# Performance work log

Measured on AMD Instinct MI355X. Metric: run time of the kernel, lower is better.

The kernel has to match this reference:

```python
import jax, jax.numpy as jnp
import numpy as np

N = 1048576          # total octree nodes across the batch
C = 64               # in_channels
BATCH_SIZE = 16
GROUP = 16           # clamped: min_group_channels(4)*group(32) > 64 -> group = 64//4
CPG = C // GROUP     # channels_per_group = 4
EPS = 1e-5


def setup_inputs() -> dict:
    key = jax.random.key(0)
    k1, k2, k3, k4 = jax.random.split(key, 4)
    data = jax.random.normal(k1, (N, C), dtype=jnp.float32)
    batch_id = jnp.sort(jax.random.randint(k2, (N,), 0, BATCH_SIZE)).astype(jnp.int32)
    weights = jax.random.normal(k3, (1, C), dtype=jnp.float32)
    bias = jax.random.normal(k4, (1, C), dtype=jnp.float32)
    return {"data": data, "batch_id": batch_id, "weights": weights, "bias": bias}


def _adjust_for_group(t):
    # sum over channels within each group, broadcast back to all channels
    if CPG > 1:
        t = t.reshape(-1, GROUP, CPG).sum(-1, keepdims=True)
        t = jnp.broadcast_to(t, (t.shape[0], GROUP, CPG)).reshape(-1, C)
    return t


def reference(data, batch_id, weights, bias):
    # per-sample element counts, scaled so the group-sum of means is a true group mean
    ones = jnp.ones((data.shape[0],), dtype=data.dtype)
    count = jax.ops.segment_sum(ones, batch_id, num_segments=BATCH_SIZE)[:, None]  # [B,1]
    count = count * CPG
    inv_count = 1.0 / (count + EPS)

    mean = jax.ops.segment_sum(data, batch_id, num_segments=BATCH_SIZE) * inv_count  # [B,C]
    mean = _adjust_for_group(mean)
    out = data - mean[batch_id]  # gather broadcast [N,C]

    var = jax.ops.segment_sum(out * out, batch_id, num_segments=BATCH_SIZE) * inv_count
    var = _adjust_for_group(var)
    inv_std = jax.lax.rsqrt(var + EPS)

    out = out * inv_std[batch_id]
    return out * weights + bias
```

## Files before the change

kernel.cpp:

```cpp
#include <hip/hip_runtime.h>

#define NBATCH 16
#define NCH 64
#define CPG 4
#define NGRP 16
#define EPSV 1e-5f

typedef float f32x4 __attribute__((ext_vector_type(4)));


__global__ void ogn_stats(const float* __restrict__ data,
                          const int* __restrict__ bid,
                          float* __restrict__ S1,
                          float* __restrict__ S2,
                          int* __restrict__ cnt,
                          int N, int rows_per_block) {
    __shared__ float ls1[NBATCH * NCH];
    __shared__ float ls2[NBATCH * NCH];
    __shared__ int   lcnt[NBATCH];

    for (int i = threadIdx.x; i < NBATCH * NCH; i += blockDim.x) {
        ls1[i] = 0.f;
        ls2[i] = 0.f;
    }
    if (threadIdx.x < NBATCH) lcnt[threadIdx.x] = 0;
    __syncthreads();

    const int t     = threadIdx.x;
    const int c4    = t & 15;
    const int rlane = t >> 4;

    long long row_begin = (long long)blockIdx.x * rows_per_block;
    long long row_end   = row_begin + rows_per_block;
    if (row_end > N) row_end = N;

    const float4* data4 = (const float4*)data;

    float4 s1 = make_float4(0.f, 0.f, 0.f, 0.f);
    float4 s2 = make_float4(0.f, 0.f, 0.f, 0.f);
    int cur = -1;
    int c   = 0;

#define FLUSH() do { if (cur >= 0) {                                   \
        int base_ = cur * NCH + c4 * 4;                                \
        atomicAdd(&ls1[base_ + 0], s1.x);                              \
        atomicAdd(&ls1[base_ + 1], s1.y);                              \
        atomicAdd(&ls1[base_ + 2], s1.z);                              \
        atomicAdd(&ls1[base_ + 3], s1.w);                              \
        atomicAdd(&ls2[base_ + 0], s2.x);                              \
        atomicAdd(&ls2[base_ + 1], s2.y);                              \
        atomicAdd(&ls2[base_ + 2], s2.z);                              \
        atomicAdd(&ls2[base_ + 3], s2.w);                              \
        if (c4 == 0) atomicAdd(&lcnt[cur], c);                         \
    } } while (0)

#define ACCV(vv) do {                                                  \
        s1.x += (vv).x; s1.y += (vv).y; s1.z += (vv).z; s1.w += (vv).w;\
        s2.x = fmaf((vv).x, (vv).x, s2.x);                             \
        s2.y = fmaf((vv).y, (vv).y, s2.y);                             \
        s2.z = fmaf((vv).z, (vv).z, s2.z);                             \
        s2.w = fmaf((vv).w, (vv).w, s2.w);                             \
    } while (0)

#define ACC1(bb, vv) do {                                              \
        if ((bb) != cur) {                                             \
            FLUSH();                                                   \
            s1 = make_float4(0.f, 0.f, 0.f, 0.f);                      \
            s2 = make_float4(0.f, 0.f, 0.f, 0.f);                      \
            c = 0; cur = (bb);                                         \
        }                                                              \
        ACCV(vv); c++;                                                 \
    } while (0)

    long long r = row_begin + rlane;

    for (; r + 48 < row_end; r += 64) {
        int b0 = bid[r];
        int b1 = bid[r + 16];
        int b2 = bid[r + 32];
        int b3 = bid[r + 48];
        float4 v0 = data4[r * 16 + c4];
        float4 v1 = data4[(r + 16) * 16 + c4];
        float4 v2 = data4[(r + 32) * 16 + c4];
        float4 v3 = data4[(r + 48) * 16 + c4];
        if (((b0 == cur) & (b1 == cur) & (b2 == cur) & (b3 == cur)) != 0) {
            ACCV(v0); ACCV(v1); ACCV(v2); ACCV(v3);
            c += 4;
        } else {
            ACC1(b0, v0);
            ACC1(b1, v1);
            ACC1(b2, v2);
            ACC1(b3, v3);
        }
    }
    for (; r < row_end; r += 16) {
        int b = bid[r];
        float4 v = data4[r * 16 + c4];
        ACC1(b, v);
    }
    FLUSH();
    __syncthreads();

    for (int i = threadIdx.x; i < NBATCH * NCH; i += blockDim.x) {
        float v1 = ls1[i];
        float v2 = ls2[i];
        if (v1 != 0.f) atomicAdd(&S1[i], v1);
        if (v2 != 0.f) atomicAdd(&S2[i], v2);
    }
    if (threadIdx.x < NBATCH) {
        int v = lcnt[threadIdx.x];
        if (v != 0) atomicAdd(&cnt[threadIdx.x], v);
    }

#undef ACC1
#undef ACCV
#undef FLUSH
}

__global__ void ogn_apply(const float* __restrict__ data,
                          const int* __restrict__ bid,
                          const float* __restrict__ S1,
                          const float* __restrict__ S2,
                          const int* __restrict__ cnt,
                          const float* __restrict__ w,
                          const float* __restrict__ bias,
                          float* __restrict__ out,
                          long long total4) {
    __shared__ float4 lA[NBATCH * NGRP];
    __shared__ float4 lB[NBATCH * NGRP];

    const int t = threadIdx.x;
    if (t < NBATCH * NGRP) {
        int b = t >> 4;
        int g = t & 15;
        int base = b * NCH + g * CPG;
        float s1g = 0.f, s2g = 0.f;
#pragma unroll
        for (int k = 0; k < CPG; ++k) {
            s1g += S1[base + k];
            s2g += S2[base + k];
        }
        float countf    = (float)cnt[b] * (float)CPG;
        float inv_count = 1.f / (countf + EPSV);
        float mean      = s1g * inv_count;
        float var       = inv_count * (s2g - 2.f * mean * s1g + countf * mean * mean);
        float inv_std   = rsqrtf(var + EPSV);

        float4 wv = ((const float4*)w)[g];
        float4 bv = ((const float4*)bias)[g];
        float4 a4, b4;
        a4.x = inv_std * wv.x; b4.x = bv.x - mean * a4.x;
        a4.y = inv_std * wv.y; b4.y = bv.y - mean * a4.y;
        a4.z = inv_std * wv.z; b4.z = bv.z - mean * a4.z;
        a4.w = inv_std * wv.w; b4.w = bv.w - mean * a4.w;
        lA[b * NGRP + g] = a4;
        lB[b * NGRP + g] = b4;
    }
    __syncthreads();

    const float4* d4 = (const float4*)data;
    float4* o4 = (float4*)out;

    long long i      = (long long)blockIdx.x * blockDim.x + threadIdx.x;
    long long stride = (long long)gridDim.x * blockDim.x;

    for (; i < total4; i += stride) {
        long long j   = total4 - 1 - i;
        long long row = j >> 4;
        int c4 = (int)(j & 15);
        int b  = bid[row];
        float4 v  = d4[j];
        float4 a  = lA[b * NGRP + c4];
        float4 bb = lB[b * NGRP + c4];
        f32x4 r;
        r.x = fmaf(v.x, a.x, bb.x);
        r.y = fmaf(v.y, a.y, bb.y);
        r.z = fmaf(v.z, a.z, bb.z);
        r.w = fmaf(v.w, a.w, bb.w);
        __builtin_nontemporal_store(r, (f32x4*)&o4[j]);
    }
}

extern "C" void kernel_launch(void* const* d_in, const int* in_sizes, int n_in,
                              void* d_out, int out_size, void* d_ws, size_t ws_size,
                              hipStream_t stream) {
    const float* data = (const float*)d_in[0];
    const int*   bid  = (const int*)d_in[1];
    const float* w    = (const float*)d_in[2];
    const float* bias = (const float*)d_in[3];
    float* out = (float*)d_out;

    int N = in_sizes[1];

    char* ws = (char*)d_ws;
    float* S1  = (float*)(ws + 0);
    float* S2  = (float*)(ws + 4096);
    int*   cnt = (int*)  (ws + 8192);

    hipMemsetAsync(d_ws, 0, 8256, stream);

    const int NB1 = 2048;
    int rows_per_block = (N + NB1 - 1) / NB1;
    ogn_stats<<<NB1, 256, 0, stream>>>(data, bid, S1, S2, cnt, N, rows_per_block);

    long long total4 = (long long)N * (NCH / 4);
    const int NB3 = 4096;
    ogn_apply<<<NB3, 256, 0, stream>>>(data, bid, S1, S2, cnt, w, bias, out, total4);
}
```

Before: 502.0 us.

## Fuse stats and apply into one cooperative kernel with grid sync

Merges the statistics and normalization kernels into a single cooperative kernel. Each block accumulates per-batch sums for its row range, the grid synchronizes, and then the same block normalizes its own rows. The aim is to remove the second kernel launch and improve cache reuse of each block's data slice. The cost is a grid-wide barrier, a single-wave grid of 1024 blocks, and a simpler, non-unrolled apply loop.

```diff
diff --git a/kernel.cpp b/kernel.cpp
--- a/kernel.cpp
+++ b/kernel.cpp
@@ -1,4 +1,7 @@
 #include <hip/hip_runtime.h>
+#include <hip/hip_cooperative_groups.h>
+
+namespace cg = cooperative_groups;
 
 #define NBATCH 16
 #define NCH 64
@@ -9,15 +12,21 @@
 typedef float f32x4 __attribute__((ext_vector_type(4)));
 
 
-__global__ void ogn_stats(const float* __restrict__ data,
-                          const int* __restrict__ bid,
-                          float* __restrict__ S1,
-                          float* __restrict__ S2,
-                          int* __restrict__ cnt,
-                          int N, int rows_per_block) {
+__global__ __launch_bounds__(256, 4)
+void ogn_fused(const float* __restrict__ data,
+               const int* __restrict__ bid,
+               float* __restrict__ S1,
+               float* __restrict__ S2,
+               int* __restrict__ cnt,
+               const float* __restrict__ w,
+               const float* __restrict__ bias,
+               float* __restrict__ out,
+               int N, int rows_per_block) {
     __shared__ float ls1[NBATCH * NCH];
     __shared__ float ls2[NBATCH * NCH];
     __shared__ int   lcnt[NBATCH];
+    __shared__ float4 lA[NBATCH * NGRP];
+    __shared__ float4 lB[NBATCH * NGRP];
 
     for (int i = threadIdx.x; i < NBATCH * NCH; i += blockDim.x) {
         ls1[i] = 0.f;
@@ -32,14 +41,16 @@
 
     long long row_begin = (long long)blockIdx.x * rows_per_block;
     long long row_end   = row_begin + rows_per_block;
+    if (row_begin > N) row_begin = N;
     if (row_end > N) row_end = N;
 
     const float4* data4 = (const float4*)data;
 
-    float4 s1 = make_float4(0.f, 0.f, 0.f, 0.f);
-    float4 s2 = make_float4(0.f, 0.f, 0.f, 0.f);
-    int cur = -1;
-    int c   = 0;
+    {
+        float4 s1 = make_float4(0.f, 0.f, 0.f, 0.f);
+        float4 s2 = make_float4(0.f, 0.f, 0.f, 0.f);
+        int cur = -1;
+        int c   = 0;
 
 #define FLUSH() do { if (cur >= 0) {                                   \
         int base_ = cur * NCH + c4 * 4;                                \
@@ -72,64 +83,53 @@
         ACCV(vv); c++;                                                 \
     } while (0)
 
-    long long r = row_begin + rlane;
-
-    for (; r + 48 < row_end; r += 64) {
-        int b0 = bid[r];
-        int b1 = bid[r + 16];
-        int b2 = bid[r + 32];
-        int b3 = bid[r + 48];
-        float4 v0 = data4[r * 16 + c4];
-        float4 v1 = data4[(r + 16) * 16 + c4];
-        float4 v2 = data4[(r + 32) * 16 + c4];
-        float4 v3 = data4[(r + 48) * 16 + c4];
-        if (((b0 == cur) & (b1 == cur) & (b2 == cur) & (b3 == cur)) != 0) {
-            ACCV(v0); ACCV(v1); ACCV(v2); ACCV(v3);
-            c += 4;
-        } else {
-            ACC1(b0, v0);
-            ACC1(b1, v1);
-            ACC1(b2, v2);
-            ACC1(b3, v3);
-        }
-    }
-    for (; r < row_end; r += 16) {
-        int b = bid[r];
-        float4 v = data4[r * 16 + c4];
-        ACC1(b, v);
-    }
-    FLUSH();
-    __syncthreads();
-
-    for (int i = threadIdx.x; i < NBATCH * NCH; i += blockDim.x) {
-        float v1 = ls1[i];
-        float v2 = ls2[i];
-        if (v1 != 0.f) atomicAdd(&S1[i], v1);
-        if (v2 != 0.f) atomicAdd(&S2[i], v2);
-    }
-    if (threadIdx.x < NBATCH) {
-        int v = lcnt[threadIdx.x];
-        if (v != 0) atomicAdd(&cnt[threadIdx.x], v);
-    }
+        long long r = row_begin + rlane;
+
+        for (; r + 48 < row_end; r += 64) {
+            int b0 = bid[r];
+            int b1 = bid[r + 16];
+            int b2 = bid[r + 32];
+            int b3 = bid[r + 48];
+            float4 v0 = data4[r * 16 + c4];
+            float4 v1 = data4[(r + 16) * 16 + c4];
+            float4 v2 = data4[(r + 32) * 16 + c4];
+            float4 v3 = data4[(r + 48) * 16 + c4];
+            if (((b0 == cur) & (b1 == cur) & (b2 == cur) & (b3 == cur)) != 0) {
+                ACCV(v0); ACCV(v1); ACCV(v2); ACCV(v3);
+                c += 4;
+            } else {
+                ACC1(b0, v0);
+                ACC1(b1, v1);
+                ACC1(b2, v2);
+                ACC1(b3, v3);
+            }
+        }
+        for (; r < row_end; r += 16) {
+            int b = bid[r];
+            float4 v = data4[r * 16 + c4];
+            ACC1(b, v);
+        }
+        FLUSH();
+        __syncthreads();
 
 #undef ACC1
 #undef ACCV
 #undef FLUSH
-}
-
-__global__ void ogn_apply(const float* __restrict__ data,
-                          const int* __restrict__ bid,
-                          const float* __restrict__ S1,
-                          const float* __restrict__ S2,
-                          const int* __restrict__ cnt,
-                          const float* __restrict__ w,
-                          const float* __restrict__ bias,
-                          float* __restrict__ out,
-                          long long total4) {
-    __shared__ float4 lA[NBATCH * NGRP];
-    __shared__ float4 lB[NBATCH * NGRP];
-
-    const int t = threadIdx.x;
+
+        for (int i = threadIdx.x; i < NBATCH * NCH; i += blockDim.x) {
+            float v1 = ls1[i];
+            float v2 = ls2[i];
+            if (v1 != 0.f) atomicAdd(&S1[i], v1);
+            if (v2 != 0.f) atomicAdd(&S2[i], v2);
+        }
+        if (threadIdx.x < NBATCH) {
+            int v = lcnt[threadIdx.x];
+            if (v != 0) atomicAdd(&cnt[threadIdx.x], v);
+        }
+    }
+
+    cg::this_grid().sync();
+
     if (t < NBATCH * NGRP) {
         int b = t >> 4;
         int g = t & 15;
@@ -137,10 +137,11 @@
         float s1g = 0.f, s2g = 0.f;
 #pragma unroll
         for (int k = 0; k < CPG; ++k) {
-            s1g += S1[base + k];
-            s2g += S2[base + k];
-        }
-        float countf    = (float)cnt[b] * (float)CPG;
+            s1g += __hip_atomic_load(&S1[base + k], __ATOMIC_RELAXED, __HIP_MEMORY_SCOPE_AGENT);
+            s2g += __hip_atomic_load(&S2[base + k], __ATOMIC_RELAXED, __HIP_MEMORY_SCOPE_AGENT);
+        }
+        int   cntb      = __hip_atomic_load(&cnt[b], __ATOMIC_RELAXED, __HIP_MEMORY_SCOPE_AGENT);
+        float countf    = (float)cntb * (float)CPG;
         float inv_count = 1.f / (countf + EPSV);
         float mean      = s1g * inv_count;
         float var       = inv_count * (s2g - 2.f * mean * s1g + countf * mean * mean);
@@ -158,26 +159,20 @@
     }
     __syncthreads();
 
-    const float4* d4 = (const float4*)data;
-    float4* o4 = (float4*)out;
-
-    long long i      = (long long)blockIdx.x * blockDim.x + threadIdx.x;
-    long long stride = (long long)gridDim.x * blockDim.x;
-
-    for (; i < total4; i += stride) {
-        long long j   = total4 - 1 - i;
-        long long row = j >> 4;
-        int c4 = (int)(j & 15);
-        int b  = bid[row];
-        float4 v  = d4[j];
-        float4 a  = lA[b * NGRP + c4];
-        float4 bb = lB[b * NGRP + c4];
-        f32x4 r;
-        r.x = fmaf(v.x, a.x, bb.x);
-        r.y = fmaf(v.y, a.y, bb.y);
-        r.z = fmaf(v.z, a.z, bb.z);
-        r.w = fmaf(v.w, a.w, bb.w);
-        __builtin_nontemporal_store(r, (f32x4*)&o4[j]);
+    {
+        float4* o4 = (float4*)out;
+        for (long long r = row_begin + rlane; r < row_end; r += 16) {
+            int b = bid[r];
+            float4 v  = data4[r * 16 + c4];
+            float4 a  = lA[b * NGRP + c4];
+            float4 bb = lB[b * NGRP + c4];
+            f32x4 res;
+            res.x = fmaf(v.x, a.x, bb.x);
+            res.y = fmaf(v.y, a.y, bb.y);
+            res.z = fmaf(v.z, a.z, bb.z);
+            res.w = fmaf(v.w, a.w, bb.w);
+            __builtin_nontemporal_store(res, (f32x4*)&o4[r * 16 + c4]);
+        }
     }
 }
 
@@ -199,11 +194,15 @@
 
     hipMemsetAsync(d_ws, 0, 8256, stream);
 
-    const int NB1 = 2048;
-    int rows_per_block = (N + NB1 - 1) / NB1;
-    ogn_stats<<<NB1, 256, 0, stream>>>(data, bid, S1, S2, cnt, N, rows_per_block);
-
-    long long total4 = (long long)N * (NCH / 4);
-    const int NB3 = 4096;
-    ogn_apply<<<NB3, 256, 0, stream>>>(data, bid, S1, S2, cnt, w, bias, out, total4);
+    const int GRID = 1024;
+    int rows_per_block = (N + GRID - 1) / GRID;
+
+    void* args[] = {
+        (void*)&data, (void*)&bid,
+        (void*)&S1, (void*)&S2, (void*)&cnt,
+        (void*)&w, (void*)&bias, (void*)&out,
+        (void*)&N, (void*)&rows_per_block
+    };
+    hipLaunchCooperativeKernel((void*)ogn_fused, dim3(GRID), dim3(256),
+                               args, 0, stream);
 }
```

Result: slower. 593.9 us (+18.3%).

## Fuse stats and apply into one cooperative kernel with grid sync

Applied to the files above, without the earlier changes.

Merges the statistics and normalize-apply kernels into one cooperative kernel that uses a grid-wide barrier. Each block applies the normalization to the same rows it just reduced, so those rows may still be in L2 or the infinity cache when they are read a second time. A fallback keeps the two-kernel path if the cooperative launch fails. The grid size comes from an occupancy query, and the grid-sync cost and lower occupancy under launch bounds are the trade-off.

```diff
diff --git a/kernel.cpp b/kernel.cpp
--- a/kernel.cpp
+++ b/kernel.cpp
@@ -1,4 +1,7 @@
 #include <hip/hip_runtime.h>
+#include <hip/hip_cooperative_groups.h>
+
+namespace cg = cooperative_groups;
 
 #define NBATCH 16
 #define NCH 64
@@ -9,15 +12,22 @@
 typedef float f32x4 __attribute__((ext_vector_type(4)));
 
 
-__global__ void ogn_stats(const float* __restrict__ data,
-                          const int* __restrict__ bid,
-                          float* __restrict__ S1,
-                          float* __restrict__ S2,
-                          int* __restrict__ cnt,
-                          int N, int rows_per_block) {
-    __shared__ float ls1[NBATCH * NCH];
-    __shared__ float ls2[NBATCH * NCH];
-    __shared__ int   lcnt[NBATCH];
+__global__ __launch_bounds__(256, 8)
+void ogn_fused(const float* __restrict__ data,
+               const int* __restrict__ bid,
+               float* __restrict__ S1,
+               float* __restrict__ S2,
+               int* __restrict__ cnt,
+               const float* __restrict__ w,
+               const float* __restrict__ bias,
+               float* __restrict__ out,
+               int N, int rows_per_block) {
+    __shared__ float4 lsA[NBATCH * NGRP];
+    __shared__ float4 lsB[NBATCH * NGRP];
+    __shared__ int    lcnt[NBATCH];
+
+    float* ls1 = (float*)lsA;
+    float* ls2 = (float*)lsB;
 
     for (int i = threadIdx.x; i < NBATCH * NCH; i += blockDim.x) {
         ls1[i] = 0.f;
@@ -32,14 +42,16 @@
 
     long long row_begin = (long long)blockIdx.x * rows_per_block;
     long long row_end   = row_begin + rows_per_block;
+    if (row_begin > N) row_begin = N;
     if (row_end > N) row_end = N;
 
     const float4* data4 = (const float4*)data;
 
-    float4 s1 = make_float4(0.f, 0.f, 0.f, 0.f);
-    float4 s2 = make_float4(0.f, 0.f, 0.f, 0.f);
-    int cur = -1;
-    int c   = 0;
+    {
+        float4 s1 = make_float4(0.f, 0.f, 0.f, 0.f);
+        float4 s2 = make_float4(0.f, 0.f, 0.f, 0.f);
+        int cur = -1;
+        int c   = 0;
 
 #define FLUSH() do { if (cur >= 0) {                                   \
         int base_ = cur * NCH + c4 * 4;                                \
@@ -72,33 +84,191 @@
         ACCV(vv); c++;                                                 \
     } while (0)
 
-    long long r = row_begin + rlane;
-
-    for (; r + 48 < row_end; r += 64) {
-        int b0 = bid[r];
-        int b1 = bid[r + 16];
-        int b2 = bid[r + 32];
-        int b3 = bid[r + 48];
-        float4 v0 = data4[r * 16 + c4];
-        float4 v1 = data4[(r + 16) * 16 + c4];
-        float4 v2 = data4[(r + 32) * 16 + c4];
-        float4 v3 = data4[(r + 48) * 16 + c4];
-        if (((b0 == cur) & (b1 == cur) & (b2 == cur) & (b3 == cur)) != 0) {
-            ACCV(v0); ACCV(v1); ACCV(v2); ACCV(v3);
-            c += 4;
-        } else {
-            ACC1(b0, v0);
-            ACC1(b1, v1);
-            ACC1(b2, v2);
-            ACC1(b3, v3);
-        }
-    }
-    for (; r < row_end; r += 16) {
+        long long r = row_begin + rlane;
+
+        for (; r + 48 < row_end; r += 64) {
+            int b0 = bid[r];
+            int b1 = bid[r + 16];
+            int b2 = bid[r + 32];
+            int b3 = bid[r + 48];
+            float4 v0 = data4[r * 16 + c4];
+            float4 v1 = data4[(r + 16) * 16 + c4];
+            float4 v2 = data4[(r + 32) * 16 + c4];
+            float4 v3 = data4[(r + 48) * 16 + c4];
+            if (((b0 == cur) & (b1 == cur) & (b2 == cur) & (b3 == cur)) != 0) {
+                ACCV(v0); ACCV(v1); ACCV(v2); ACCV(v3);
+                c += 4;
+            } else {
+                ACC1(b0, v0);
+                ACC1(b1, v1);
+                ACC1(b2, v2);
+                ACC1(b3, v3);
+            }
+        }
+        for (; r < row_end; r += 16) {
+            int b = bid[r];
+            float4 v = data4[r * 16 + c4];
+            ACC1(b, v);
+        }
+        FLUSH();
+        __syncthreads();
+
+#undef ACC1
+#undef ACCV
+#undef FLUSH
+
+        for (int i = threadIdx.x; i < NBATCH * NCH; i += blockDim.x) {
+            float v1 = ls1[i];
+            float v2 = ls2[i];
+            if (v1 != 0.f) atomicAdd(&S1[i], v1);
+            if (v2 != 0.f) atomicAdd(&S2[i], v2);
+        }
+        if (threadIdx.x < NBATCH) {
+            int v = lcnt[threadIdx.x];
+            if (v != 0) atomicAdd(&cnt[threadIdx.x], v);
+        }
+    }
+
+    cg::this_grid().sync();
+
+    if (t < NBATCH * NGRP) {
+        int b = t >> 4;
+        int g = t & 15;
+        int base = b * NCH + g * CPG;
+        float s1g = 0.f, s2g = 0.f;
+#pragma unroll
+        for (int k = 0; k < CPG; ++k) {
+            s1g += __hip_atomic_load(&S1[base + k], __ATOMIC_RELAXED, __HIP_MEMORY_SCOPE_AGENT);
+            s2g += __hip_atomic_load(&S2[base + k], __ATOMIC_RELAXED, __HIP_MEMORY_SCOPE_AGENT);
+        }
+        int   cntb      = __hip_atomic_load(&cnt[b], __ATOMIC_RELAXED, __HIP_MEMORY_SCOPE_AGENT);
+        float countf    = (float)cntb * (float)CPG;
+        float inv_count = 1.f / (countf + EPSV);
+        float mean      = s1g * inv_count;
+        float var       = inv_count * (s2g - 2.f * mean * s1g + countf * mean * mean);
+        float inv_std   = rsqrtf(var + EPSV);
+
+        float4 wv = ((const float4*)w)[g];
+        float4 bv = ((const float4*)bias)[g];
+        float4 a4, b4;
+        a4.x = inv_std * wv.x; b4.x = bv.x - mean * a4.x;
+        a4.y = inv_std * wv.y; b4.y = bv.y - mean * a4.y;
+        a4.z = inv_std * wv.z; b4.z = bv.z - mean * a4.z;
+        a4.w = inv_std * wv.w; b4.w = bv.w - mean * a4.w;
+        lsA[b * NGRP + g] = a4;
+        lsB[b * NGRP + g] = b4;
+    }
+    __syncthreads();
+
+    {
+        float4* o4 = (float4*)out;
+        long long r = row_begin + rlane;
+        for (; r + 48 < row_end; r += 64) {
+            int b0 = bid[r];
+            int b1 = bid[r + 16];
+            int b2 = bid[r + 32];
+            int b3 = bid[r + 48];
+            float4 v0 = data4[r * 16 + c4];
+            float4 v1 = data4[(r + 16) * 16 + c4];
+            float4 v2 = data4[(r + 32) * 16 + c4];
+            float4 v3 = data4[(r + 48) * 16 + c4];
+#define APPLY1(rr, bb, vv) do {                                        \
+            float4 a_  = lsA[(bb) * NGRP + c4];                        \
+            float4 b_  = lsB[(bb) * NGRP + c4];                        \
+            f32x4 res_;                                                \
+            res_.x = fmaf((vv).x, a_.x, b_.x);                         \
+            res_.y = fmaf((vv).y, a_.y, b_.y);                         \
+            res_.z = fmaf((vv).z, a_.z, b_.z);                         \
+            res_.w = fmaf((vv).w, a_.w, b_.w);                         \
+            __builtin_nontemporal_store(res_, (f32x4*)&o4[(rr) * 16 + c4]); \
+        } while (0)
+            APPLY1(r, b0, v0);
+            APPLY1(r + 16, b1, v1);
+            APPLY1(r + 32, b2, v2);
+            APPLY1(r + 48, b3, v3);
+        }
+        for (; r < row_end; r += 16) {
+            int b = bid[r];
+            float4 v = data4[r * 16 + c4];
+            APPLY1(r, b, v);
+        }
+#undef APPLY1
+    }
+}
+
+__global__ void ogn_stats_fb(const float* __restrict__ data,
+                             const int* __restrict__ bid,
+                             float* __restrict__ S1,
+                             float* __restrict__ S2,
+                             int* __restrict__ cnt,
+                             int N, int rows_per_block) {
+    __shared__ float ls1[NBATCH * NCH];
+    __shared__ float ls2[NBATCH * NCH];
+    __shared__ int   lcnt[NBATCH];
+
+    for (int i = threadIdx.x; i < NBATCH * NCH; i += blockDim.x) {
+        ls1[i] = 0.f;
+        ls2[i] = 0.f;
+    }
+    if (threadIdx.x < NBATCH) lcnt[threadIdx.x] = 0;
+    __syncthreads();
+
+    const int t     = threadIdx.x;
+    const int c4    = t & 15;
+    const int rlane = t >> 4;
+
+    long long row_begin = (long long)blockIdx.x * rows_per_block;
+    long long row_end   = row_begin + rows_per_block;
+    if (row_begin > N) row_begin = N;
+    if (row_end > N) row_end = N;
+
+    const float4* data4 = (const float4*)data;
+
+    float4 s1 = make_float4(0.f, 0.f, 0.f, 0.f);
+    float4 s2 = make_float4(0.f, 0.f, 0.f, 0.f);
+    int cur = -1;
+    int c   = 0;
+
+    for (long long r = row_begin + rlane; r < row_end; r += 16) {
         int b = bid[r];
+        if (b != cur) {
+            if (cur >= 0) {
+                int base = cur * NCH + c4 * 4;
+                atomicAdd(&ls1[base + 0], s1.x);
+                atomicAdd(&ls1[base + 1], s1.y);
+                atomicAdd(&ls1[base + 2], s1.z);
+                atomicAdd(&ls1[base + 3], s1.w);
+                atomicAdd(&ls2[base + 0], s2.x);
+                atomicAdd(&ls2[base + 1], s2.y);
+                atomicAdd(&ls2[base + 2], s2.z);
+                atomicAdd(&ls2[base + 3], s2.w);
+                if (c4 == 0) atomicAdd(&lcnt[cur], c);
+            }
+            s1 = make_float4(0.f, 0.f, 0.f, 0.f);
+            s2 = make_float4(0.f, 0.f, 0.f, 0.f);
+            c = 0;
+            cur = b;
+        }
         float4 v = data4[r * 16 + c4];
-        ACC1(b, v);
-    }
-    FLUSH();
+        s1.x += v.x; s1.y += v.y; s1.z += v.z; s1.w += v.w;
+        s2.x = fmaf(v.x, v.x, s2.x);
+        s2.y = fmaf(v.y, v.y, s2.y);
+        s2.z = fmaf(v.z, v.z, s2.z);
+        s2.w = fmaf(v.w, v.w, s2.w);
+        c++;
+    }
+    if (cur >= 0) {
+        int base = cur * NCH + c4 * 4;
+        atomicAdd(&ls1[base + 0], s1.x);
+        atomicAdd(&ls1[base + 1], s1.y);
+        atomicAdd(&ls1[base + 2], s1.z);
+        atomicAdd(&ls1[base + 3], s1.w);
+        atomicAdd(&ls2[base + 0], s2.x);
+        atomicAdd(&ls2[base + 1], s2.y);
+        atomicAdd(&ls2[base + 2], s2.z);
+        atomicAdd(&ls2[base + 3], s2.w);
+        if (c4 == 0) atomicAdd(&lcnt[cur], c);
+    }
     __syncthreads();
 
     for (int i = threadIdx.x; i < NBATCH * NCH; i += blockDim.x) {
@@ -111,21 +281,17 @@
         int v = lcnt[threadIdx.x];
         if (v != 0) atomicAdd(&cnt[threadIdx.x], v);
     }
-
-#undef ACC1
-#undef ACCV
-#undef FLUSH
 }
 
-__global__ void ogn_apply(const float* __restrict__ data,
-                          const int* __restrict__ bid,
-                          const float* __restrict__ S1,
-                          const float* __restrict__ S2,
-                          const int* __restrict__ cnt,
-                          const float* __restrict__ w,
-                          const float* __restrict__ bias,
-                          float* __restrict__ out,
-                          long long total4) {
+__global__ void ogn_apply_fb(const float* __restrict__ data,
+                             const int* __restrict__ bid,
+                             const float* __restrict__ S1,
+                             const float* __restrict__ S2,
+                             const int* __restrict__ cnt,
+                             const float* __restrict__ w,
+                             const float* __restrict__ bias,
+                             float* __restrict__ out,
+                             long long total4) {
     __shared__ float4 lA[NBATCH * NGRP];
     __shared__ float4 lB[NBATCH * NGRP];
 
@@ -199,11 +365,39 @@
 
     hipMemsetAsync(d_ws, 0, 8256, stream);
 
-    const int NB1 = 2048;
-    int rows_per_block = (N + NB1 - 1) / NB1;
-    ogn_stats<<<NB1, 256, 0, stream>>>(data, bid, S1, S2, cnt, N, rows_per_block);
-
-    long long total4 = (long long)N * (NCH / 4);
-    const int NB3 = 4096;
-    ogn_apply<<<NB3, 256, 0, stream>>>(data, bid, S1, S2, cnt, w, bias, out, total4);
+    static int s_grid = -1;
+    if (s_grid < 0) {
+        int maxB = 0;
+        hipError_t e1 = hipOccupancyMaxActiveBlocksPerMultiprocessor(
+            &maxB, (const void*)ogn_fused, 256, 0);
+        hipDeviceProp_t prop;
+        hipError_t e2 = hipGetDeviceProperties(&prop, 0);
+        if (e1 == hipSuccess && e2 == hipSuccess && maxB > 0)
+            s_grid = maxB * prop.multiProcessorCount;
+        else
+            s_grid = 0;
+    }
+
+    bool done = false;
+    if (s_grid >= 256) {
+        int grid = s_grid;
+        int rows_per_block = (int)((N + (long long)grid - 1) / grid);
+        void* args[] = {
+            (void*)&data, (void*)&bid,
+            (void*)&S1, (void*)&S2, (void*)&cnt,
+            (void*)&w, (void*)&bias, (void*)&out,
+            (void*)&N, (void*)&rows_per_block
+        };
+        hipError_t e = hipLaunchCooperativeKernel((void*)ogn_fused, dim3(grid),
+                                                  dim3(256), args, 0, stream);
+        done = (e == hipSuccess);
+    }
+
+    if (!done) {
+        const int NB1 = 2048;
+        int rows_per_block = (N + NB1 - 1) / NB1;
+        ogn_stats_fb<<<NB1, 256, 0, stream>>>(data, bid, S1, S2, cnt, N, rows_per_block);
+        long long total4 = (long long)N * (NCH / 4);
+        ogn_apply_fb<<<4096, 256, 0, stream>>>(data, bid, S1, S2, cnt, w, bias, out, total4);
+    }
 }
```

Result: slower. 582.4 us (+16.0%).
